# Kernel tuning notes

Measured on AMD Instinct MI355X. Metric: run time of the kernel, lower is better.

Reference implementation:

```python
import jax, jax.numpy as jnp
import numpy as np

EMBED_DIM = 32
HIDDEN_DIM = 64
N = 1024
LN_EPS = 1e-5


def setup_inputs() -> dict:
    key = jax.random.key(0)
    ks = jax.random.split(key, 8)
    d, h = EMBED_DIM, HIDDEN_DIM
    s1 = 1.0 / np.sqrt(2 * d)
    s2 = 1.0 / np.sqrt(h)
    return {
        "node_embeddings": jax.random.normal(ks[0], (N, d), dtype=jnp.float32),
        # Linear(2d -> h), stored as (2d, h) for x @ W
        "W1": jax.random.uniform(ks[1], (2 * d, h), jnp.float32, -s1, s1),
        "b1": jnp.zeros((h,), jnp.float32),
        "g1": jnp.ones((h,), jnp.float32),
        "be1": jnp.zeros((h,), jnp.float32),
        "W2": jax.random.uniform(ks[2], (h, h), jnp.float32, -s2, s2),
        "b2": jnp.zeros((h,), jnp.float32),
        "g2": jnp.ones((h,), jnp.float32),
        "be2": jnp.zeros((h,), jnp.float32),
        "W3": jax.random.uniform(ks[3], (h, 1), jnp.float32, -s2, s2),
        "b3": jnp.zeros((1,), jnp.float32),
    }


def _layernorm(x, gamma, beta):
    mu = jnp.mean(x, axis=-1, keepdims=True)
    var = jnp.mean(jnp.square(x - mu), axis=-1, keepdims=True)
    return (x - mu) * jax.lax.rsqrt(var + LN_EPS) * gamma + beta


def reference(node_embeddings, W1, b1, g1, be1, W2, b2, g2, be2, W3, b3):
    n, d = node_embeddings.shape
    # pair_emb = cat([src_emb, dst_emb], -1); first linear applied without
    # materializing the concat: split W1 into src/dst halves.
    W1s, W1d = W1[:d], W1[d:]
    hs = node_embeddings @ W1s          # (N, h)
    hd = node_embeddings @ W1d          # (N, h)
    h = hs[:, None, :] + hd[None, :, :] + b1   # (N, N, h)
    h = jax.nn.relu(_layernorm(h, g1, be1))
    h = jax.nn.relu(_layernorm(h @ W2 + b2, g2, be2))
    out = jax.nn.sigmoid((h @ W3 + b3)[..., 0])  # (N, N)
    return out
```

## Files before the change

### kernel.cpp

```cpp
#include <hip/hip_runtime.h>
#include <hip/hip_bf16.h>

#define NN 1024
#define ED 32
#define HD 64
#define LN_EPS 1e-5f

typedef short bf16x8 __attribute__((ext_vector_type(8)));
typedef float f32x4 __attribute__((ext_vector_type(4)));

#define OFF_HS   0
#define OFF_HDB  65536
#define OFF_SS   131072
#define OFF_SD   132096
#define OFF_G1   133120
#define OFF_BE1  133184
#define OFF_B2   133248
#define OFF_G2   133312
#define OFF_BE2  133376
#define OFF_W3   133440
#define OFF_B3   133504
#define OFF_SB2  133505
#define OFF_W2F  133508

__device__ __forceinline__ bool buf_is_f32(const void* g1) {
  return *(const unsigned int*)g1 == 0x3F800000u;
}
template <bool F32>
__device__ __forceinline__ float ld(const void* p, int i) {
  return F32 ? ((const float*)p)[i]
             : __bfloat162float(((const __hip_bfloat16*)p)[i]);
}
__device__ __forceinline__ unsigned short f2bf(float f) {
  unsigned int b = __builtin_bit_cast(unsigned int, f);
  b += 0x7FFFu + ((b >> 16) & 1u);
  return (unsigned short)(b >> 16);
}
__device__ __forceinline__ unsigned int pack2bf(float a, float b) {
  return (unsigned int)f2bf(a) | ((unsigned int)f2bf(b) << 16);
}
__device__ __forceinline__ unsigned int pk_bf(float a, float b) {
  __hip_bfloat162 p = __float22bfloat162_rn(make_float2(a, b));
  unsigned int u;
  __builtin_memcpy(&u, &p, 4);
  return u;
}
__device__ __forceinline__ f32x4 splat4(float v) { f32x4 r = {v, v, v, v}; return r; }

template <int CTRL>
__device__ __forceinline__ float dpp_add(float v) {
  int m = __builtin_amdgcn_update_dpp(0, __builtin_bit_cast(int, v), CTRL, 0xF, 0xF, true);
  return v + __builtin_bit_cast(float, m);
}
__device__ __forceinline__ float red16(float v) {
  v = dpp_add<0xB1>(v);
  v = dpp_add<0x4E>(v);
  v = dpp_add<0x124>(v);
  v = dpp_add<0x128>(v);
  return v;
}

template <bool F32>
__device__ void prep_body(const void* E, const void* W1, const void* b1,
                          const void* g1, const void* be1, const void* W2,
                          const void* b2, const void* g2, const void* be2,
                          const void* W3, const void* b3, float* ws) {
  const int i = blockIdx.x, t = threadIdx.x;
  if (i < NN) {
    __shared__ float e[ED];
    if (t < ED) e[t] = ld<F32>(E, i * ED + t);
    __syncthreads();
    int k = t & 63;
    bool dside = t >= 64;
    int wofs = dside ? ED * HD : 0;
    float acc = 0.f;
#pragma unroll
    for (int c = 0; c < ED; ++c)
      acc = fmaf(e[c], ld<F32>(W1, wofs + c * HD + k), acc);
    if (dside) acc += ld<F32>(b1, k);
    float s = acc;
#pragma unroll
    for (int m = 1; m <= 32; m <<= 1) s += __shfl_xor(s, m);
    if (dside) {
      ws[OFF_HDB + i * HD + k] = acc;
      if (k == 0) ws[OFF_SD + i] = s;
    } else {
      ws[OFF_HS + i * HD + k] = acc;
      if (k == 0) ws[OFF_SS + i] = s;
    }
  } else if (i < NN + 16) {
    if (t < 32) {
      int d = (i - NN) * 32 + t;
      int lv = d & 63, nt = (d >> 6) & 3, kc = d >> 8;
      int k0 = kc * 32 + ((lv >> 4) & 3) * 8;
      int n = nt * 16 + (lv & 15);
      unsigned int u4[4];
#pragma unroll
      for (int jj = 0; jj < 4; ++jj)
        u4[jj] = pack2bf(ld<F32>(W2, (k0 + 2 * jj) * HD + n),
                         ld<F32>(W2, (k0 + 2 * jj + 1) * HD + n));
      ((uint4*)(ws + OFF_W2F))[d] = make_uint4(u4[0], u4[1], u4[2], u4[3]);
    }
  } else {
    __shared__ float rs[64];
    if (t < 64) {
      ws[OFF_G1  + t] = ld<F32>(g1,  t);
      ws[OFF_BE1 + t] = ld<F32>(be1, t);
      ws[OFF_B2  + t] = ld<F32>(b2,  t);
      ws[OFF_G2  + t] = ld<F32>(g2,  t);
      ws[OFF_BE2 + t] = ld<F32>(be2, t);
      ws[OFF_W3  + t] = ld<F32>(W3,  t);
      float s = 0.f;
      for (int n = 0; n < HD; ++n) s += ld<F32>(W2, t * HD + n);
      rs[t] = s;
    }
    if (t == 64) {
      float s = 0.f;
      for (int n = 0; n < HD; ++n) s += ld<F32>(b2, n);
      ws[OFF_SB2] = s;
    }
    if (t == 65) ws[OFF_B3] = ld<F32>(b3, 0);
    __syncthreads();
    unsigned short* st = (unsigned short*)(ws + OFF_W2F) + 4096;
    for (int s = t; s < 1024; s += 128) {
      int j = s & 7, lv = (s >> 3) & 63, kc = s >> 9;
      st[s] = f2bf(rs[kc * 32 + ((lv >> 4) & 3) * 8 + j]);
    }
  }
}

__global__ __launch_bounds__(128) void prep_kern(
    const void* E, const void* W1, const void* b1, const void* g1,
    const void* be1, const void* W2, const void* b2, const void* g2,
    const void* be2, const void* W3, const void* b3, float* ws) {
  if (buf_is_f32(g1))
    prep_body<true >(E, W1, b1, g1, be1, W2, b2, g2, be2, W3, b3, ws);
  else
    prep_body<false>(E, W1, b1, g1, be1, W2, b2, g2, be2, W3, b3, ws);
}

__global__ __launch_bounds__(256, 4) void pair_kern(
    const float* __restrict__ ws, float* __restrict__ out) {
  __shared__ float sh[1024];
  __shared__ float sdt[1024];
  __shared__ __align__(16) unsigned int X[256 * 32];
  const int t = threadIdx.x;
  const int bi = blockIdx.y, bj = blockIdx.x;
  const int l = t & 63, w = t >> 6;
  const int q = l >> 4, ln = l & 15;
  const float inv = 1.f / 64.f;

  {
    int r = t >> 4, c4 = t & 15;
    ((f32x4*)sh )[r * 16 + (c4 ^ r)] = ((const f32x4*)(ws + OFF_HS  + (bi * 16 + r) * HD))[c4];
    ((f32x4*)sdt)[r * 16 + (c4 ^ r)] = ((const f32x4*)(ws + OFF_HDB + (bj * 16 + r) * HD))[c4];
  }
  const int il = t >> 4, jl = t & 15;
  const float ssum = ws[OFF_SS + bi * 16 + il];
  const float dsum = ws[OFF_SD + bj * 16 + jl];
  __syncthreads();

  {
    const f32x4* A4 = (const f32x4*)sh;
    const f32x4* B4 = (const f32x4*)sdt;
    f32x4 xv[16];
    f32x4 q4 = splat4(0.f);
#pragma unroll
    for (int c = 0; c < 16; ++c) {
      f32x4 x = A4[il * 16 + (c ^ il)] + B4[jl * 16 + (c ^ jl)];
      xv[c] = x;
      q4 = __builtin_elementwise_fma(x, x, q4);
    }
    float ssq = (q4[0] + q4[1]) + (q4[2] + q4[3]);
    float mu = (ssum + dsum) * inv;
    float r1 = rsqrtf(fmaf(-mu, mu, ssq * inv) + LN_EPS);
    f32x4 r1v = splat4(r1), nm = splat4(-mu * r1), zero = splat4(0.f);
    uint4* Xr4 = (uint4*)(X + t * 32);
#pragma unroll
    for (int b = 0; b < 8; ++b) {
      unsigned int uu[4];
#pragma unroll
      for (int h = 0; h < 2; ++h) {
        int c = 2 * b + h;
        f32x4 g, be;
#pragma unroll
        for (int e = 0; e < 4; ++e) {
          g[e]  = ws[OFF_G1  + c * 4 + e];
          be[e] = ws[OFF_BE1 + c * 4 + e];
        }
        f32x4 u = __builtin_elementwise_fma(xv[c], r1v, nm);
        f32x4 v = __builtin_elementwise_fma(u, g, be);
        v = __builtin_elementwise_max(v, zero);
        uu[2 * h]     = pk_bf(v[0], v[1]);
        uu[2 * h + 1] = pk_bf(v[2], v[3]);
      }
      Xr4[b ^ (t & 7)] = make_uint4(uu[0], uu[1], uu[2], uu[3]);
    }
  }

  bf16x8 bf[2][4], bsum[2];
  const uint4* WF4 = (const uint4*)(ws + OFF_W2F);
#pragma unroll
  for (int kc = 0; kc < 2; ++kc) {
#pragma unroll
    for (int nt = 0; nt < 4; ++nt)
      bf[kc][nt] = __builtin_bit_cast(bf16x8, WF4[(kc * 4 + nt) * 64 + l]);
    bsum[kc] = __builtin_bit_cast(bf16x8, WF4[512 + kc * 64 + l]);
  }
  f32x4 acc[4][5];
  const uint4* XL = (const uint4*)X;
#pragma unroll
  for (int mt = 0; mt < 4; ++mt) {
    int m = w * 64 + mt * 16 + ln;
    bf16x8 a0 = __builtin_bit_cast(bf16x8, XL[m * 8 + (q ^ (m & 7))]);
    bf16x8 a1 = __builtin_bit_cast(bf16x8, XL[m * 8 + ((q + 4) ^ (m & 7))]);
#pragma unroll
    for (int nt = 0; nt < 5; ++nt) {
      bf16x8 b0  = (nt < 4) ? bf[0][nt] : bsum[0];
      bf16x8 b1f = (nt < 4) ? bf[1][nt] : bsum[1];
      f32x4 z4 = splat4(0.f);
      z4 = __builtin_amdgcn_mfma_f32_16x16x32_bf16(a0, b0, z4, 0, 0, 0);
      acc[mt][nt] = __builtin_amdgcn_mfma_f32_16x16x32_bf16(a1, b1f, z4, 0, 0, 0);
    }
  }

  float b2v[4], g2v[4], be2v[4], w3v[4];
#pragma unroll
  for (int nt = 0; nt < 4; ++nt) {
    int cix = nt * 16 + ln;
    b2v[nt]  = ws[OFF_B2  + cix];
    g2v[nt]  = ws[OFF_G2  + cix];
    be2v[nt] = ws[OFF_BE2 + cix];
    w3v[nt]  = ws[OFF_W3  + cix];
  }
  const float b3s = ws[OFF_B3];
  const float Sb2 = ws[OFF_SB2];

#pragma unroll
  for (int mt = 0; mt < 4; ++mt) {
    f32x4 y[4], qq = splat4(0.f);
#pragma unroll
    for (int nt = 0; nt < 4; ++nt) {
      y[nt] = acc[mt][nt] + splat4(b2v[nt]);
      qq = __builtin_elementwise_fma(y[nt], y[nt], qq);
    }
#pragma unroll
    for (int e = 0; e < 4; ++e) qq[e] = red16(qq[e]);
    f32x4 s4 = acc[mt][4] + splat4(Sb2);
    f32x4 mu = s4 * inv;
    f32x4 var = qq * inv - mu * mu;
    f32x4 r2;
#pragma unroll
    for (int e = 0; e < 4; ++e) r2[e] = rsqrtf(var[e] + LN_EPS);
    f32x4 z4 = splat4(0.f);
#pragma unroll
    for (int nt = 0; nt < 4; ++nt) {
      f32x4 u = (y[nt] - mu) * r2;
      f32x4 v = __builtin_elementwise_fma(u, splat4(g2v[nt]), splat4(be2v[nt]));
      v = __builtin_elementwise_max(v, splat4(0.f));
      z4 = __builtin_elementwise_fma(v, splat4(w3v[nt]), z4);
    }
#pragma unroll
    for (int e = 0; e < 4; ++e) z4[e] = red16(z4[e]);
    float z01 = (ln & 1) ? z4[1] : z4[0];
    float z23 = (ln & 1) ? z4[3] : z4[2];
    float zs = ((ln & 2) ? z23 : z01) + b3s;
    float o = 1.f / (1.f + __expf(-zs));
    if (ln < 4)
      out[(bi * 16 + w * 4 + mt) * NN + bj * 16 + q * 4 + ln] = o;
  }
}

extern "C" void kernel_launch(void* const* d_in, const int* in_sizes, int n_in,
                              void* d_out, int out_size, void* d_ws, size_t ws_size,
                              hipStream_t stream) {
  float* ws = (float*)d_ws;
  hipLaunchKernelGGL(prep_kern, dim3(NN + 17), dim3(128), 0, stream,
                     d_in[0], d_in[1], d_in[2], d_in[3], d_in[4], d_in[5],
                     d_in[6], d_in[7], d_in[8], d_in[9], d_in[10], ws);
  hipLaunchKernelGGL(pair_kern, dim3(64, 64), dim3(256), 0, stream,
                     ws, (float*)d_out);
}
```

Before: 119.5 us.

## Read hs/hd rows directly from global, interleave MFMA with epilogue per tile

The pair kernel no longer stages the hs/hd rows through swizzled shared memory with a block barrier. Each thread now reads its own 64-float rows straight from global memory, relying on cache for reuse across the 16 threads that share a row. The MFMA accumulation is moved into the per-tile epilogue loop, so only 5 accumulators are live at a time instead of 20, which lowers register pressure. The prep kernel's W2 row-sum is split across two threads per row, combined with a shuffle.

Result: slower. 155.3 us (+30.0%).

```diff
diff --git a/kernel.cpp b/kernel.cpp
--- a/kernel.cpp
+++ b/kernel.cpp
@@ -110,9 +110,16 @@
       ws[OFF_G2  + t] = ld<F32>(g2,  t);
       ws[OFF_BE2 + t] = ld<F32>(be2, t);
       ws[OFF_W3  + t] = ld<F32>(W3,  t);
+    }
+    {
+      int row = t >> 1;
+      int half = t & 1;
       float s = 0.f;
-      for (int n = 0; n < HD; ++n) s += ld<F32>(W2, t * HD + n);
-      rs[t] = s;
+#pragma unroll
+      for (int n = 0; n < 32; ++n)
+        s += ld<F32>(W2, row * HD + half * 32 + n);
+      s += __shfl_xor(s, 1);
+      if (half == 0) rs[row] = s;
     }
     if (t == 64) {
       float s = 0.f;
@@ -141,33 +148,24 @@
 
 __global__ __launch_bounds__(256, 4) void pair_kern(
     const float* __restrict__ ws, float* __restrict__ out) {
-  __shared__ float sh[1024];
-  __shared__ float sdt[1024];
   __shared__ __align__(16) unsigned int X[256 * 32];
   const int t = threadIdx.x;
   const int bi = blockIdx.y, bj = blockIdx.x;
   const int l = t & 63, w = t >> 6;
   const int q = l >> 4, ln = l & 15;
+  const int il = t >> 4, jl = t & 15;
   const float inv = 1.f / 64.f;
 
   {
-    int r = t >> 4, c4 = t & 15;
-    ((f32x4*)sh )[r * 16 + (c4 ^ r)] = ((const f32x4*)(ws + OFF_HS  + (bi * 16 + r) * HD))[c4];
-    ((f32x4*)sdt)[r * 16 + (c4 ^ r)] = ((const f32x4*)(ws + OFF_HDB + (bj * 16 + r) * HD))[c4];
-  }
-  const int il = t >> 4, jl = t & 15;
-  const float ssum = ws[OFF_SS + bi * 16 + il];
-  const float dsum = ws[OFF_SD + bj * 16 + jl];
-  __syncthreads();
-
-  {
-    const f32x4* A4 = (const f32x4*)sh;
-    const f32x4* B4 = (const f32x4*)sdt;
+    const f32x4* A4 = (const f32x4*)(ws + OFF_HS  + (bi * 16 + il) * HD);
+    const f32x4* B4 = (const f32x4*)(ws + OFF_HDB + (bj * 16 + jl) * HD);
+    const float ssum = ws[OFF_SS + bi * 16 + il];
+    const float dsum = ws[OFF_SD + bj * 16 + jl];
     f32x4 xv[16];
     f32x4 q4 = splat4(0.f);
 #pragma unroll
     for (int c = 0; c < 16; ++c) {
-      f32x4 x = A4[il * 16 + (c ^ il)] + B4[jl * 16 + (c ^ jl)];
+      f32x4 x = A4[c] + B4[c];
       xv[c] = x;
       q4 = __builtin_elementwise_fma(x, x, q4);
     }
@@ -207,23 +205,6 @@
       bf[kc][nt] = __builtin_bit_cast(bf16x8, WF4[(kc * 4 + nt) * 64 + l]);
     bsum[kc] = __builtin_bit_cast(bf16x8, WF4[512 + kc * 64 + l]);
   }
-  f32x4 acc[4][5];
-  const uint4* XL = (const uint4*)X;
-#pragma unroll
-  for (int mt = 0; mt < 4; ++mt) {
-    int m = w * 64 + mt * 16 + ln;
-    bf16x8 a0 = __builtin_bit_cast(bf16x8, XL[m * 8 + (q ^ (m & 7))]);
-    bf16x8 a1 = __builtin_bit_cast(bf16x8, XL[m * 8 + ((q + 4) ^ (m & 7))]);
-#pragma unroll
-    for (int nt = 0; nt < 5; ++nt) {
-      bf16x8 b0  = (nt < 4) ? bf[0][nt] : bsum[0];
-      bf16x8 b1f = (nt < 4) ? bf[1][nt] : bsum[1];
-      f32x4 z4 = splat4(0.f);
-      z4 = __builtin_amdgcn_mfma_f32_16x16x32_bf16(a0, b0, z4, 0, 0, 0);
-      acc[mt][nt] = __builtin_amdgcn_mfma_f32_16x16x32_bf16(a1, b1f, z4, 0, 0, 0);
-    }
-  }
-
   float b2v[4], g2v[4], be2v[4], w3v[4];
 #pragma unroll
   for (int nt = 0; nt < 4; ++nt) {
@@ -235,18 +216,32 @@
   }
   const float b3s = ws[OFF_B3];
   const float Sb2 = ws[OFF_SB2];
+  const uint4* XL = (const uint4*)X;
 
 #pragma unroll
   for (int mt = 0; mt < 4; ++mt) {
+    int m = w * 64 + mt * 16 + ln;
+    bf16x8 a0 = __builtin_bit_cast(bf16x8, XL[m * 8 + (q ^ (m & 7))]);
+    bf16x8 a1 = __builtin_bit_cast(bf16x8, XL[m * 8 + ((q + 4) ^ (m & 7))]);
+    f32x4 acc[5];
+#pragma unroll
+    for (int nt = 0; nt < 5; ++nt) {
+      bf16x8 b0  = (nt < 4) ? bf[0][nt] : bsum[0];
+      bf16x8 b1f = (nt < 4) ? bf[1][nt] : bsum[1];
+      f32x4 z4 = splat4(0.f);
+      z4 = __builtin_amdgcn_mfma_f32_16x16x32_bf16(a0, b0, z4, 0, 0, 0);
+      acc[nt] = __builtin_amdgcn_mfma_f32_16x16x32_bf16(a1, b1f, z4, 0, 0, 0);
+    }
+
     f32x4 y[4], qq = splat4(0.f);
 #pragma unroll
     for (int nt = 0; nt < 4; ++nt) {
-      y[nt] = acc[mt][nt] + splat4(b2v[nt]);
+      y[nt] = acc[nt] + splat4(b2v[nt]);
       qq = __builtin_elementwise_fma(y[nt], y[nt], qq);
     }
 #pragma unroll
     for (int e = 0; e < 4; ++e) qq[e] = red16(qq[e]);
-    f32x4 s4 = acc[mt][4] + splat4(Sb2);
+    f32x4 s4 = acc[4] + splat4(Sb2);
     f32x4 mu = s4 * inv;
     f32x4 var = qq * inv - mu * mu;
     f32x4 r2;
```
